# Kernel optimization log

Hardware: AMD Instinct MI355X
Metric: run time of the kernel (lower is better)

The kernel has to match this reference:

```python
import jax, jax.numpy as jnp
import numpy as np


def _gcn_conv(x, edge_index, W, b):
    """PyG-style GCNConv: h = x @ W; out = D^-1/2 (A+I) D^-1/2 h + b."""
    N = x.shape[0]
    h = x @ W  # [N, F_out]
    # add self loops
    loops = jnp.arange(N, dtype=edge_index.dtype)
    src = jnp.concatenate([edge_index[0], loops])  # [E+N]
    dst = jnp.concatenate([edge_index[1], loops])  # [E+N]
    # symmetric normalization based on in-degree (incl. self loops)
    deg = jnp.zeros((N,), dtype=h.dtype).at[dst].add(1.0)
    dinv = jnp.where(deg > 0, jax.lax.rsqrt(deg), 0.0)
    norm = dinv[src] * dinv[dst]  # [E+N]
    # gather -> scale -> scatter-add
    msgs = h[src] * norm[:, None]  # [E+N, F_out]
    out = jax.ops.segment_sum(msgs, dst, num_segments=N)
    return out + b


def setup_inputs() -> dict:
    key = jax.random.key(0)
    k1, k2, k3, k4 = jax.random.split(key, 4)
    N, E, Cin, Ch, Cout = 50000, 800000, 128, 128, 64
    x = jax.random.normal(k1, (N, Cin), dtype=jnp.float32)
    edge_index = jax.random.randint(k2, (2, E), 0, N, dtype=jnp.int64)
    W1 = jax.random.normal(k3, (Cin, Ch), dtype=jnp.float32) / np.sqrt(Cin)
    b1 = jnp.zeros((Ch,), dtype=jnp.float32)
    W2 = jax.random.normal(k4, (Ch, Cout), dtype=jnp.float32) / np.sqrt(Ch)
    b2 = jnp.zeros((Cout,), dtype=jnp.float32)
    return {"x": x, "edge_index": edge_index, "W1": W1, "b1": b1, "W2": W2, "b2": b2}


def reference(x, edge_index, W1, b1, W2, b2):
    h = jax.nn.relu(_gcn_conv(x, edge_index, W1, b1))
    # F.dropout(training=self.training): eval mode -> identity
    return _gcn_conv(h, edge_index, W2, b2)
```

## Files before the change

### kernel.cpp

```cpp
#include <hip/hip_runtime.h>

typedef _Float16 f16;
typedef f16 f16x2 __attribute__((ext_vector_type(2)));
typedef f16 f16x8 __attribute__((ext_vector_type(8)));
typedef float f32x4 __attribute__((ext_vector_type(4)));

#define BSH 7
#define BN 128
#define CHUNK 4096
#define LCAP 4096
#define NBMAX 512

__global__ __launch_bounds__(256) void k1(const float* __restrict__ x,
                                          const float* __restrict__ W1,
                                          const int* __restrict__ dst, f16* __restrict__ h,
                                          int* __restrict__ histG, int N, int E, int NB,
                                          int nblk) {
    __shared__ int hist[NBMAX];
    __shared__ f16 aT[64 * 136];
    __shared__ f16 bT[128 * 136];
    const int t = threadIdx.x;

    if ((int)blockIdx.x < nblk) {
        const int blk = blockIdx.x;
        for (int i = t; i < NB; i += 256) hist[i] = 0;
        __syncthreads();
        int lo = blk * CHUNK, hi = min(lo + CHUNK, E);
        for (int i = lo + t; i < hi; i += 256) atomicAdd(&hist[dst[i] >> BSH], 1);
        __syncthreads();
        for (int i = t; i < NB; i += 256) histG[(size_t)i * nblk + blk] = hist[i];
        return;
    }

    const int gb = blockIdx.x - nblk;
    const int row0 = gb * 64;
    {
        int r = t >> 2, s = (t & 3) * 32;
        bool ok = (row0 + r) < N;
        const float* xp = x + (size_t)(row0 + r) * 128 + s;
        f16* dp = &aT[r * 136 + s];
#pragma unroll
        for (int c = 0; c < 4; ++c) {
            f16x8 hv;
            if (ok) {
                float4 f0 = *(const float4*)(xp + c * 8);
                float4 f1 = *(const float4*)(xp + c * 8 + 4);
                hv[0] = (f16)f0.x; hv[1] = (f16)f0.y; hv[2] = (f16)f0.z; hv[3] = (f16)f0.w;
                hv[4] = (f16)f1.x; hv[5] = (f16)f1.y; hv[6] = (f16)f1.z; hv[7] = (f16)f1.w;
            } else {
#pragma unroll
                for (int j = 0; j < 8; ++j) hv[j] = (f16)0.f;
            }
            *(f16x8*)(dp + c * 8) = hv;
        }
    }
    for (int idx = t; idx < 128 * 128; idx += 256) {
        int k = idx >> 7, n = idx & 127;
        bT[n * 136 + k] = (f16)W1[idx];
    }
    __syncthreads();

    const int w = t >> 6, lane = t & 63, m15 = lane & 15, quad = lane >> 4;
    f32x4 acc[8];
#pragma unroll
    for (int c = 0; c < 8; ++c) acc[c] = (f32x4){0.f, 0.f, 0.f, 0.f};
    const f16* ar = &aT[(w * 16 + m15) * 136 + quad * 8];
#pragma unroll
    for (int k0 = 0; k0 < 128; k0 += 32) {
        f16x8 a = *(const f16x8*)(ar + k0);
#pragma unroll
        for (int c = 0; c < 8; ++c) {
            f16x8 b = *(const f16x8*)(&bT[(c * 16 + m15) * 136 + k0 + quad * 8]);
            acc[c] = __builtin_amdgcn_mfma_f32_16x16x32_f16(a, b, acc[c], 0, 0, 0);
        }
    }
#pragma unroll
    for (int c = 0; c < 8; ++c)
#pragma unroll
        for (int r = 0; r < 4; ++r) {
            int row = row0 + w * 16 + quad * 4 + r;
            if (row < N) h[(size_t)row * 128 + c * 16 + m15] = (f16)acc[c][r];
        }
}

__global__ __launch_bounds__(256) void scanA(int* __restrict__ a, int* __restrict__ bsum, int L) {
    __shared__ int tmp[256];
    int tid = threadIdx.x;
    int i = blockIdx.x * 256 + tid;
    int v = (i < L) ? a[i] : 0;
    tmp[tid] = v;
    __syncthreads();
    for (int o = 1; o < 256; o <<= 1) {
        int t2 = (tid >= o) ? tmp[tid - o] : 0;
        __syncthreads();
        tmp[tid] += t2;
        __syncthreads();
    }
    if (i < L) a[i] = tmp[tid] - v;
    if (tid == 255) bsum[blockIdx.x] = tmp[255];
}

__global__ __launch_bounds__(512) void scanB(int* __restrict__ bsum, int nb,
                                             int* __restrict__ rowstart, int N, int E) {
    __shared__ int tmp[512];
    int tid = threadIdx.x;
    int v = (tid < nb) ? bsum[tid] : 0;
    tmp[tid] = v;
    __syncthreads();
    for (int o = 1; o < 512; o <<= 1) {
        int t2 = (tid >= o) ? tmp[tid - o] : 0;
        __syncthreads();
        tmp[tid] += t2;
        __syncthreads();
    }
    if (tid < nb) bsum[tid] = tmp[tid] - v;
    if (tid == 0) rowstart[N] = E;
}

__global__ __launch_bounds__(256) void place(const int* __restrict__ src,
                                             const int* __restrict__ dst,
                                             const int* __restrict__ histG,
                                             const int* __restrict__ bsumS,
                                             int* __restrict__ sorted, int E, int NB, int nblk) {
    __shared__ int ofs[NBMAX];
    const int t = threadIdx.x, blk = blockIdx.x;
    for (int i = t; i < NB; i += 256) {
        int idx = i * nblk + blk;
        ofs[i] = histG[idx] + bsumS[idx >> 8];
    }
    __syncthreads();
    int lo = blk * CHUNK, hi = min(lo + CHUNK, E);
    for (int i = lo + t; i < hi; i += 256) {
        int d = dst[i];
        int pos = atomicAdd(&ofs[d >> BSH], 1);
        sorted[pos] = (src[i] << BSH) | (d & (BN - 1));
    }
}

__global__ __launch_bounds__(256) void bucket_build(const int* __restrict__ histG,
                                                    const int* __restrict__ bsumS,
                                                    const int* __restrict__ sorted,
                                                    int* __restrict__ rowstart,
                                                    float* __restrict__ dinv,
                                                    int* __restrict__ csr_src, int N, int E,
                                                    int NB, int nblk) {
    __shared__ int ent[LCAP];
    __shared__ int hist[BN];
    __shared__ int lofs[BN];
    const int b = blockIdx.x, t = threadIdx.x;

    const int i0 = b * nblk;
    const int base = histG[i0] + bsumS[i0 >> 8];
    const int endb = (b == NB - 1) ? E : (histG[i0 + nblk] + bsumS[(i0 + nblk) >> 8]);
    int total = min(endb - base, LCAP);

    for (int i = t; i < total; i += 256) ent[i] = sorted[base + i];
    if (t < BN) hist[t] = 0;
    __syncthreads();
    for (int i = t; i < total; i += 256) atomicAdd(&hist[ent[i] & (BN - 1)], 1);
    __syncthreads();
    if (t < BN) lofs[t] = hist[t];
    __syncthreads();
    for (int o = 1; o < BN; o <<= 1) {
        int v = (t < BN && t >= o) ? lofs[t - o] : 0;
        __syncthreads();
        if (t < BN) lofs[t] += v;
        __syncthreads();
    }
    if (t < BN) {
        int excl = lofs[t] - hist[t];
        int node = (b << BSH) + t;
        if (node < N) {
            rowstart[node] = base + excl;
            dinv[node] = rsqrtf((float)hist[t] + 1.0f);
        }
        lofs[t] = excl;
    }
    __syncthreads();
    for (int i = t; i < total; i += 256) {
        int e = ent[i];
        int pos = atomicAdd(&lofs[e & (BN - 1)], 1);
        csr_src[base + pos] = e >> BSH;
    }
}

__global__ __launch_bounds__(256) void gather1(const int* __restrict__ rowstart,
                                               const int* __restrict__ csr_src,
                                               const float* __restrict__ dinv,
                                               const f16* __restrict__ h,
                                               const float* __restrict__ b1,
                                               f16* __restrict__ r1, int N) {
    int node = (blockIdx.x * 256 + threadIdx.x) >> 6;
    int lane = threadIdx.x & 63;
    if (node >= N) return;
    int beg = rowstart[node], end = rowstart[node + 1];
    float dn = dinv[node];
    const f16x2* hv = (const f16x2*)h;

    f16x2 sv = hv[(size_t)node * 64 + lane];
    float ax = dn * (float)sv[0], ay = dn * (float)sv[1];
    int i = beg;
    for (; i + 4 <= end; i += 4) {
        int s0 = csr_src[i], s1 = csr_src[i + 1], s2 = csr_src[i + 2], s3 = csr_src[i + 3];
        float w0 = dinv[s0], w1 = dinv[s1], w2 = dinv[s2], w3 = dinv[s3];
        f16x2 v0 = hv[(size_t)s0 * 64 + lane];
        f16x2 v1 = hv[(size_t)s1 * 64 + lane];
        f16x2 v2 = hv[(size_t)s2 * 64 + lane];
        f16x2 v3 = hv[(size_t)s3 * 64 + lane];
        ax = fmaf(w0, (float)v0[0], ax); ay = fmaf(w0, (float)v0[1], ay);
        ax = fmaf(w1, (float)v1[0], ax); ay = fmaf(w1, (float)v1[1], ay);
        ax = fmaf(w2, (float)v2[0], ax); ay = fmaf(w2, (float)v2[1], ay);
        ax = fmaf(w3, (float)v3[0], ax); ay = fmaf(w3, (float)v3[1], ay);
    }
    for (; i < end; ++i) {
        int s = csr_src[i];
        float w = dinv[s];
        f16x2 v = hv[(size_t)s * 64 + lane];
        ax = fmaf(w, (float)v[0], ax);
        ay = fmaf(w, (float)v[1], ay);
    }
    float2 bb = ((const float2*)b1)[lane];
    float ox = fmaxf(fmaf(dn, ax, bb.x), 0.f);
    float oy = fmaxf(fmaf(dn, ay, bb.y), 0.f);
    ((f16x2*)r1)[(size_t)node * 64 + lane] = (f16x2){(f16)ox, (f16)oy};
}

__global__ __launch_bounds__(256) void gemm2(const f16* __restrict__ r1,
                                             const float* __restrict__ W2, f16* __restrict__ h2,
                                             int N) {
    __shared__ f16 aT[64 * 136];
    __shared__ f16 bT[64 * 136];
    const int t = threadIdx.x;
    const int row0 = blockIdx.x * 64;
    {
        int r = t >> 2, s = (t & 3) * 32;
        bool ok = (row0 + r) < N;
        const f16* rp = r1 + (size_t)(row0 + r) * 128 + s;
        f16* dp = &aT[r * 136 + s];
#pragma unroll
        for (int c = 0; c < 4; ++c) {
            f16x8 hv;
            if (ok) hv = *(const f16x8*)(rp + c * 8);
            else {
#pragma unroll
                for (int j = 0; j < 8; ++j) hv[j] = (f16)0.f;
            }
            *(f16x8*)(dp + c * 8) = hv;
        }
    }
    for (int idx = t; idx < 128 * 64; idx += 256) {
        int k = idx >> 6, n = idx & 63;
        bT[n * 136 + k] = (f16)W2[idx];
    }
    __syncthreads();

    const int w = t >> 6, lane = t & 63, m15 = lane & 15, quad = lane >> 4;
    f32x4 acc[4];
#pragma unroll
    for (int c = 0; c < 4; ++c) acc[c] = (f32x4){0.f, 0.f, 0.f, 0.f};
    const f16* ar = &aT[(w * 16 + m15) * 136 + quad * 8];
#pragma unroll
    for (int k0 = 0; k0 < 128; k0 += 32) {
        f16x8 a = *(const f16x8*)(ar + k0);
#pragma unroll
        for (int c = 0; c < 4; ++c) {
            f16x8 b = *(const f16x8*)(&bT[(c * 16 + m15) * 136 + k0 + quad * 8]);
            acc[c] = __builtin_amdgcn_mfma_f32_16x16x32_f16(a, b, acc[c], 0, 0, 0);
        }
    }
#pragma unroll
    for (int c = 0; c < 4; ++c)
#pragma unroll
        for (int r = 0; r < 4; ++r) {
            int row = row0 + w * 16 + quad * 4 + r;
            if (row < N) h2[(size_t)row * 64 + c * 16 + m15] = (f16)acc[c][r];
        }
}

__global__ __launch_bounds__(256) void gather2(const int* __restrict__ rowstart,
                                               const int* __restrict__ csr_src,
                                               const float* __restrict__ dinv,
                                               const f16* __restrict__ h2,
                                               const float* __restrict__ b2,
                                               float* __restrict__ out, int N) {
    int node = (blockIdx.x * 256 + threadIdx.x) >> 6;
    int lane = threadIdx.x & 63;
    if (node >= N) return;
    int beg = rowstart[node], end = rowstart[node + 1];
    float dn = dinv[node];

    float a = dn * (float)h2[(size_t)node * 64 + lane];
    int i = beg;
    for (; i + 4 <= end; i += 4) {
        int s0 = csr_src[i], s1 = csr_src[i + 1], s2 = csr_src[i + 2], s3 = csr_src[i + 3];
        float w0 = dinv[s0], w1 = dinv[s1], w2 = dinv[s2], w3 = dinv[s3];
        float v0 = (float)h2[(size_t)s0 * 64 + lane];
        float v1 = (float)h2[(size_t)s1 * 64 + lane];
        float v2 = (float)h2[(size_t)s2 * 64 + lane];
        float v3 = (float)h2[(size_t)s3 * 64 + lane];
        a = fmaf(w0, v0, a);
        a = fmaf(w1, v1, a);
        a = fmaf(w2, v2, a);
        a = fmaf(w3, v3, a);
    }
    for (; i < end; ++i) {
        int s = csr_src[i];
        a = fmaf(dinv[s], (float)h2[(size_t)s * 64 + lane], a);
    }
    out[(size_t)node * 64 + lane] = fmaf(dn, a, b2[lane]);
}

extern "C" void kernel_launch(void* const* d_in, const int* in_sizes, int n_in,
                              void* d_out, int out_size, void* d_ws, size_t ws_size,
                              hipStream_t stream) {
    const float* x  = (const float*)d_in[0];
    const int*   ei = (const int*)d_in[1];
    const float* W1 = (const float*)d_in[2];
    const float* b1 = (const float*)d_in[3];
    const float* W2 = (const float*)d_in[4];
    const float* b2 = (const float*)d_in[5];

    const int N = in_sizes[0] / 128;
    const int E = in_sizes[1] / 2;
    const int* src = ei;
    const int* dst = ei + E;
    const int NB   = (N + BN - 1) >> BSH;
    const int nblk = (E + CHUNK - 1) / CHUNK;
    const int L    = NB * nblk;
    const int nb2  = (L + 255) / 256;

    char* p = (char*)d_ws;
    auto bump = [&](size_t bytes) {
        char* r = p;
        p += (bytes + 255) & ~(size_t)255;
        return r;
    };
    int*   histG    = (int*)bump((size_t)L * 4);
    int*   bsum     = (int*)bump((size_t)nb2 * 4);
    int*   sorted   = (int*)bump((size_t)E * 4);
    int*   rowstart = (int*)bump((size_t)(N + 1) * 4);
    float* dinv     = (float*)bump((size_t)N * 4);
    int*   csr_src  = (int*)bump((size_t)E * 4);
    f16*   h        = (f16*)bump((size_t)N * 128 * 2);
    f16*   r1       = (f16*)bump((size_t)N * 128 * 2);
    f16*   h2       = (f16*)bump((size_t)N * 64 * 2);
    float* out      = (float*)d_out;

    k1<<<nblk + (N + 63) / 64, 256, 0, stream>>>(x, W1, dst, h, histG, N, E, NB, nblk);
    scanA<<<nb2, 256, 0, stream>>>(histG, bsum, L);
    scanB<<<1, 512, 0, stream>>>(bsum, nb2, rowstart, N, E);
    place<<<nblk, 256, 0, stream>>>(src, dst, histG, bsum, sorted, E, NB, nblk);
    bucket_build<<<NB, 256, 0, stream>>>(histG, bsum, sorted, rowstart, dinv, csr_src, N, E, NB,
                                         nblk);
    gather1<<<(N + 3) / 4, 256, 0, stream>>>(rowstart, csr_src, dinv, h, b1, r1, N);
    gemm2<<<(N + 63) / 64, 256, 0, stream>>>(r1, W2, h2, N);
    gather2<<<(N + 3) / 4, 256, 0, stream>>>(rowstart, csr_src, dinv, h2, b2, out, N);
}
```

Baseline: 204.1 us.

## Fuse layer-1 gather with second GEMM and fold partial-sum scan into consumers

Removes the scanB kernel launch by having every place and bucket_build block redundantly scan the block-sum partials in shared memory. Fuses gather1 and gemm2 into one 1024-thread kernel: each of 16 waves aggregates one node into a shared-memory tile, then four waves run MFMA against W2. This drops the r1 intermediate's global round trip and two launches. In exchange, each block reconverts W2 to f16 in LDS (one block per 16 nodes, so many times over), uses only 4 of 16 waves for the MFMA step, and repeats the scan in every block.

Measured after the change: 205.8 us. No clear change (+0.9%).

```diff
diff --git a/kernel.cpp b/kernel.cpp
--- a/kernel.cpp
+++ b/kernel.cpp
@@ -10,6 +10,7 @@
 #define CHUNK 4096
 #define LCAP 4096
 #define NBMAX 512
+#define PMAX 512
 
 __global__ __launch_bounds__(256) void k1(const float* __restrict__ x,
                                           const float* __restrict__ W1,
@@ -100,33 +101,36 @@
     if (tid == 255) bsum[blockIdx.x] = tmp[255];
 }
 
-__global__ __launch_bounds__(512) void scanB(int* __restrict__ bsum, int nb,
-                                             int* __restrict__ rowstart, int N, int E) {
-    __shared__ int tmp[512];
-    int tid = threadIdx.x;
-    int v = (tid < nb) ? bsum[tid] : 0;
-    tmp[tid] = v;
-    __syncthreads();
-    for (int o = 1; o < 512; o <<= 1) {
-        int t2 = (tid >= o) ? tmp[tid - o] : 0;
-        __syncthreads();
-        tmp[tid] += t2;
-        __syncthreads();
-    }
-    if (tid < nb) bsum[tid] = tmp[tid] - v;
-    if (tid == 0) rowstart[N] = E;
+__device__ __forceinline__ void scan_partials(const int* __restrict__ bsum, int nb2,
+                                              int* excl , int* work ) {
+    const int t = threadIdx.x & 255;
+#pragma unroll
+    for (int i = t; i < PMAX; i += 256) work[i] = (i < nb2) ? bsum[i] : 0;
+    __syncthreads();
+    for (int o = 1; o < PMAX; o <<= 1) {
+        for (int i = t; i < PMAX; i += 256)
+            excl[i] = work[i] + ((i >= o) ? work[i - o] : 0);
+        __syncthreads();
+        for (int i = t; i < PMAX; i += 256) work[i] = excl[i];
+        __syncthreads();
+    }
+    for (int i = t; i < PMAX; i += 256) excl[i] = (i == 0) ? 0 : work[i - 1];
+    __syncthreads();
 }
 
 __global__ __launch_bounds__(256) void place(const int* __restrict__ src,
                                              const int* __restrict__ dst,
                                              const int* __restrict__ histG,
-                                             const int* __restrict__ bsumS,
+                                             const int* __restrict__ bsum, int nb2,
                                              int* __restrict__ sorted, int E, int NB, int nblk) {
+    __shared__ int excl[PMAX];
+    __shared__ int work[PMAX];
     __shared__ int ofs[NBMAX];
     const int t = threadIdx.x, blk = blockIdx.x;
+    scan_partials(bsum, nb2, excl, work);
     for (int i = t; i < NB; i += 256) {
         int idx = i * nblk + blk;
-        ofs[i] = histG[idx] + bsumS[idx >> 8];
+        ofs[i] = histG[idx] + excl[idx >> 8];
     }
     __syncthreads();
     int lo = blk * CHUNK, hi = min(lo + CHUNK, E);
@@ -138,7 +142,7 @@
 }
 
 __global__ __launch_bounds__(256) void bucket_build(const int* __restrict__ histG,
-                                                    const int* __restrict__ bsumS,
+                                                    const int* __restrict__ bsum, int nb2,
                                                     const int* __restrict__ sorted,
                                                     int* __restrict__ rowstart,
                                                     float* __restrict__ dinv,
@@ -147,12 +151,16 @@
     __shared__ int ent[LCAP];
     __shared__ int hist[BN];
     __shared__ int lofs[BN];
+    __shared__ int excl[PMAX];
+    __shared__ int work[PMAX];
     const int b = blockIdx.x, t = threadIdx.x;
+    scan_partials(bsum, nb2, excl, work);
 
     const int i0 = b * nblk;
-    const int base = histG[i0] + bsumS[i0 >> 8];
-    const int endb = (b == NB - 1) ? E : (histG[i0 + nblk] + bsumS[(i0 + nblk) >> 8]);
+    const int base = histG[i0] + excl[i0 >> 8];
+    const int endb = (b == NB - 1) ? E : (histG[i0 + nblk] + excl[(i0 + nblk) >> 8]);
     int total = min(endb - base, LCAP);
+    if (b == 0 && t == 0) rowstart[N] = E;
 
     for (int i = t; i < total; i += 256) ent[i] = sorted[base + i];
     if (t < BN) hist[t] = 0;
@@ -168,13 +176,13 @@
         __syncthreads();
     }
     if (t < BN) {
-        int excl = lofs[t] - hist[t];
+        int ex = lofs[t] - hist[t];
         int node = (b << BSH) + t;
         if (node < N) {
-            rowstart[node] = base + excl;
+            rowstart[node] = base + ex;
             dinv[node] = rsqrtf((float)hist[t] + 1.0f);
         }
-        lofs[t] = excl;
+        lofs[t] = ex;
     }
     __syncthreads();
     for (int i = t; i < total; i += 256) {
@@ -184,97 +192,75 @@
     }
 }
 
-__global__ __launch_bounds__(256) void gather1(const int* __restrict__ rowstart,
-                                               const int* __restrict__ csr_src,
-                                               const float* __restrict__ dinv,
-                                               const f16* __restrict__ h,
-                                               const float* __restrict__ b1,
-                                               f16* __restrict__ r1, int N) {
-    int node = (blockIdx.x * 256 + threadIdx.x) >> 6;
-    int lane = threadIdx.x & 63;
-    if (node >= N) return;
-    int beg = rowstart[node], end = rowstart[node + 1];
-    float dn = dinv[node];
-    const f16x2* hv = (const f16x2*)h;
-
-    f16x2 sv = hv[(size_t)node * 64 + lane];
-    float ax = dn * (float)sv[0], ay = dn * (float)sv[1];
-    int i = beg;
-    for (; i + 4 <= end; i += 4) {
-        int s0 = csr_src[i], s1 = csr_src[i + 1], s2 = csr_src[i + 2], s3 = csr_src[i + 3];
-        float w0 = dinv[s0], w1 = dinv[s1], w2 = dinv[s2], w3 = dinv[s3];
-        f16x2 v0 = hv[(size_t)s0 * 64 + lane];
-        f16x2 v1 = hv[(size_t)s1 * 64 + lane];
-        f16x2 v2 = hv[(size_t)s2 * 64 + lane];
-        f16x2 v3 = hv[(size_t)s3 * 64 + lane];
-        ax = fmaf(w0, (float)v0[0], ax); ay = fmaf(w0, (float)v0[1], ay);
-        ax = fmaf(w1, (float)v1[0], ax); ay = fmaf(w1, (float)v1[1], ay);
-        ax = fmaf(w2, (float)v2[0], ax); ay = fmaf(w2, (float)v2[1], ay);
-        ax = fmaf(w3, (float)v3[0], ax); ay = fmaf(w3, (float)v3[1], ay);
-    }
-    for (; i < end; ++i) {
-        int s = csr_src[i];
-        float w = dinv[s];
-        f16x2 v = hv[(size_t)s * 64 + lane];
-        ax = fmaf(w, (float)v[0], ax);
-        ay = fmaf(w, (float)v[1], ay);
-    }
-    float2 bb = ((const float2*)b1)[lane];
-    float ox = fmaxf(fmaf(dn, ax, bb.x), 0.f);
-    float oy = fmaxf(fmaf(dn, ay, bb.y), 0.f);
-    ((f16x2*)r1)[(size_t)node * 64 + lane] = (f16x2){(f16)ox, (f16)oy};
-}
-
-__global__ __launch_bounds__(256) void gemm2(const f16* __restrict__ r1,
-                                             const float* __restrict__ W2, f16* __restrict__ h2,
-                                             int N) {
-    __shared__ f16 aT[64 * 136];
+__global__ __launch_bounds__(1024) void g1_gemm2(const int* __restrict__ rowstart,
+                                                 const int* __restrict__ csr_src,
+                                                 const float* __restrict__ dinv,
+                                                 const f16* __restrict__ h,
+                                                 const float* __restrict__ b1,
+                                                 const float* __restrict__ W2,
+                                                 f16* __restrict__ h2, int N) {
+    __shared__ f16 r1s[16 * 136];
     __shared__ f16 bT[64 * 136];
-    const int t = threadIdx.x;
-    const int row0 = blockIdx.x * 64;
-    {
-        int r = t >> 2, s = (t & 3) * 32;
-        bool ok = (row0 + r) < N;
-        const f16* rp = r1 + (size_t)(row0 + r) * 128 + s;
-        f16* dp = &aT[r * 136 + s];
-#pragma unroll
-        for (int c = 0; c < 4; ++c) {
-            f16x8 hv;
-            if (ok) hv = *(const f16x8*)(rp + c * 8);
-            else {
-#pragma unroll
-                for (int j = 0; j < 8; ++j) hv[j] = (f16)0.f;
-            }
-            *(f16x8*)(dp + c * 8) = hv;
-        }
-    }
-    for (int idx = t; idx < 128 * 64; idx += 256) {
+    const int t = threadIdx.x, w = t >> 6, lane = t & 63;
+
+    for (int idx = t; idx < 128 * 64; idx += 1024) {
         int k = idx >> 6, n = idx & 63;
         bT[n * 136 + k] = (f16)W2[idx];
     }
-    __syncthreads();
-
-    const int w = t >> 6, lane = t & 63, m15 = lane & 15, quad = lane >> 4;
-    f32x4 acc[4];
-#pragma unroll
-    for (int c = 0; c < 4; ++c) acc[c] = (f32x4){0.f, 0.f, 0.f, 0.f};
-    const f16* ar = &aT[(w * 16 + m15) * 136 + quad * 8];
-#pragma unroll
-    for (int k0 = 0; k0 < 128; k0 += 32) {
-        f16x8 a = *(const f16x8*)(ar + k0);
-#pragma unroll
-        for (int c = 0; c < 4; ++c) {
-            f16x8 b = *(const f16x8*)(&bT[(c * 16 + m15) * 136 + k0 + quad * 8]);
-            acc[c] = __builtin_amdgcn_mfma_f32_16x16x32_f16(a, b, acc[c], 0, 0, 0);
-        }
-    }
-#pragma unroll
-    for (int c = 0; c < 4; ++c)
+
+    const int node = blockIdx.x * 16 + w;
+    if (node < N) {
+        int beg = rowstart[node], end = rowstart[node + 1];
+        float dn = dinv[node];
+        const f16x2* hv = (const f16x2*)h;
+
+        f16x2 sv = hv[(size_t)node * 64 + lane];
+        float ax = dn * (float)sv[0], ay = dn * (float)sv[1];
+        int i = beg;
+        for (; i + 4 <= end; i += 4) {
+            int s0 = csr_src[i], s1 = csr_src[i + 1], s2 = csr_src[i + 2], s3 = csr_src[i + 3];
+            float w0 = dinv[s0], w1 = dinv[s1], w2 = dinv[s2], w3 = dinv[s3];
+            f16x2 v0 = hv[(size_t)s0 * 64 + lane];
+            f16x2 v1 = hv[(size_t)s1 * 64 + lane];
+            f16x2 v2 = hv[(size_t)s2 * 64 + lane];
+            f16x2 v3 = hv[(size_t)s3 * 64 + lane];
+            ax = fmaf(w0, (float)v0[0], ax); ay = fmaf(w0, (float)v0[1], ay);
+            ax = fmaf(w1, (float)v1[0], ax); ay = fmaf(w1, (float)v1[1], ay);
+            ax = fmaf(w2, (float)v2[0], ax); ay = fmaf(w2, (float)v2[1], ay);
+            ax = fmaf(w3, (float)v3[0], ax); ay = fmaf(w3, (float)v3[1], ay);
+        }
+        for (; i < end; ++i) {
+            int s = csr_src[i];
+            float ws = dinv[s];
+            f16x2 v = hv[(size_t)s * 64 + lane];
+            ax = fmaf(ws, (float)v[0], ax);
+            ay = fmaf(ws, (float)v[1], ay);
+        }
+        float2 bb = ((const float2*)b1)[lane];
+        float ox = fmaxf(fmaf(dn, ax, bb.x), 0.f);
+        float oy = fmaxf(fmaf(dn, ay, bb.y), 0.f);
+        *(f16x2*)(&r1s[w * 136 + 2 * lane]) = (f16x2){(f16)ox, (f16)oy};
+    } else {
+        *(f16x2*)(&r1s[w * 136 + 2 * lane]) = (f16x2){(f16)0.f, (f16)0.f};
+    }
+    __syncthreads();
+
+    if (w < 4) {
+        const int m15 = lane & 15, quad = lane >> 4;
+        f32x4 acc = (f32x4){0.f, 0.f, 0.f, 0.f};
+        const f16* ar = &r1s[m15 * 136 + quad * 8];
+#pragma unroll
+        for (int k0 = 0; k0 < 128; k0 += 32) {
+            f16x8 a = *(const f16x8*)(ar + k0);
+            f16x8 b = *(const f16x8*)(&bT[(w * 16 + m15) * 136 + k0 + quad * 8]);
+            acc = __builtin_amdgcn_mfma_f32_16x16x32_f16(a, b, acc, 0, 0, 0);
+        }
 #pragma unroll
         for (int r = 0; r < 4; ++r) {
-            int row = row0 + w * 16 + quad * 4 + r;
-            if (row < N) h2[(size_t)row * 64 + c * 16 + m15] = (f16)acc[c][r];
-        }
+            int row = blockIdx.x * 16 + quad * 4 + r;
+            if (row < N) h2[(size_t)row * 64 + w * 16 + m15] = (f16)acc[r];
+        }
+    }
 }
 
 __global__ __launch_bounds__(256) void gather2(const int* __restrict__ rowstart,
@@ -342,17 +328,14 @@
     float* dinv     = (float*)bump((size_t)N * 4);
     int*   csr_src  = (int*)bump((size_t)E * 4);
     f16*   h        = (f16*)bump((size_t)N * 128 * 2);
-    f16*   r1       = (f16*)bump((size_t)N * 128 * 2);
     f16*   h2       = (f16*)bump((size_t)N * 64 * 2);
     float* out      = (float*)d_out;
 
     k1<<<nblk + (N + 63) / 64, 256, 0, stream>>>(x, W1, dst, h, histG, N, E, NB, nblk);
     scanA<<<nb2, 256, 0, stream>>>(histG, bsum, L);
-    scanB<<<1, 512, 0, stream>>>(bsum, nb2, rowstart, N, E);
-    place<<<nblk, 256, 0, stream>>>(src, dst, histG, bsum, sorted, E, NB, nblk);
-    bucket_build<<<NB, 256, 0, stream>>>(histG, bsum, sorted, rowstart, dinv, csr_src, N, E, NB,
-                                         nblk);
-    gather1<<<(N + 3) / 4, 256, 0, stream>>>(rowstart, csr_src, dinv, h, b1, r1, N);
-    gemm2<<<(N + 63) / 64, 256, 0, stream>>>(r1, W2, h2, N);
+    place<<<nblk, 256, 0, stream>>>(src, dst, histG, bsum, nb2, sorted, E, NB, nblk);
+    bucket_build<<<NB, 256, 0, stream>>>(histG, bsum, nb2, sorted, rowstart, dinv, csr_src, N, E,
+                                         NB, nblk);
+    g1_gemm2<<<(N + 15) / 16, 1024, 0, stream>>>(rowstart, csr_src, dinv, h, b1, W2, h2, N);
     gather2<<<(N + 3) / 4, 256, 0, stream>>>(rowstart, csr_src, dinv, h2, b2, out, N);
 }
```
